# Performance work log

Measured on AMD Instinct MI355X. Metric: run time of the kernel, lower is better.

The kernel has to match this reference:

```python
import jax, jax.numpy as jnp
import numpy as np

NTYPES = 2
MAXNEI = 128      # maxNeighborNum
M2 = 16
NPER = 256        # atoms per type
B = 4
EMB = [25, 50, 100]
FIT_IN = M2 * EMB[-1]  # 1600
FH = 240


def setup_inputs() -> dict:
    key = jax.random.key(0)
    ks = jax.random.split(key, 16)
    s = 0.1
    inp = {
        "Ri": jax.random.normal(ks[0], (B, NTYPES * NPER, NTYPES * MAXNEI, 4), jnp.float32),
        "emb_W0": jax.random.normal(ks[1], (4, 1, EMB[0]), jnp.float32) * s,
        "emb_b0": jax.random.normal(ks[2], (4, EMB[0]), jnp.float32) * s,
        "emb_W1": jax.random.normal(ks[3], (4, EMB[0], EMB[1]), jnp.float32) * s,
        "emb_b1": jax.random.normal(ks[4], (4, EMB[1]), jnp.float32) * s,
        "emb_W2": jax.random.normal(ks[5], (4, EMB[1], EMB[2]), jnp.float32) * s,
        "emb_b2": jax.random.normal(ks[6], (4, EMB[2]), jnp.float32) * s,
        "fit_W0": jax.random.normal(ks[7], (2, FIT_IN, FH), jnp.float32) * 0.02,
        "fit_b0": jax.random.normal(ks[8], (2, FH), jnp.float32) * s,
        "fit_W1": jax.random.normal(ks[9], (2, FH, FH), jnp.float32) * 0.05,
        "fit_b1": jax.random.normal(ks[10], (2, FH), jnp.float32) * s,
        "fit_W2": jax.random.normal(ks[11], (2, FH, FH), jnp.float32) * 0.05,
        "fit_b2": jax.random.normal(ks[12], (2, FH), jnp.float32) * s,
        "fit_W3": jax.random.normal(ks[13], (2, FH, 1), jnp.float32) * 0.05,
        "fit_b3": jax.random.normal(ks[14], (2, 1), jnp.float32),
    }
    return inp


def _emb(s, W0, b0, W1, b1, W2, b2):
    # DeepMD-style embedding MLP with doubling resnet skips (1->25->50->100)
    h0 = jnp.tanh(s @ W0 + b0)
    h1 = jnp.tanh(h0 @ W1 + b1) + jnp.concatenate([h0, h0], axis=-1)
    h2 = jnp.tanh(h1 @ W2 + b2) + jnp.concatenate([h1, h1], axis=-1)
    return h2


def _fit(d, W0, b0, W1, b1, W2, b2, W3, b3):
    h = jnp.tanh(d @ W0 + b0)
    h = jnp.tanh(h @ W1 + b1) + h   # resnet skip (equal dims)
    h = jnp.tanh(h @ W2 + b2) + h
    return h @ W3 + b3              # [B, N, 1]


def reference(Ri, emb_W0, emb_b0, emb_W1, emb_b1, emb_W2, emb_b2,
              fit_W0, fit_b0, fit_W1, fit_b1, fit_W2, fit_b2, fit_W3, fit_b3):
    type_nums = NTYPES
    Ei_blocks = []
    for i in range(NTYPES):                      # center-atom type
        Ri_i = Ri[:, i * NPER:(i + 1) * NPER]    # [B, NPER, NTYPES*M, 4]
        xyz = None
        for j in range(NTYPES):                  # neighbor type
            blk = Ri_i[:, :, j * MAXNEI:(j + 1) * MAXNEI, :]  # [B,N,M,4]
            S = blk[..., 0:1]                                  # [B,N,M,1]
            e = i * NTYPES + j
            G = _emb(S, emb_W0[e], emb_b0[e], emb_W1[e], emb_b1[e],
                     emb_W2[e], emb_b2[e])                     # [B,N,M,100]
            tmp = jnp.einsum('bnmc,bnmg->bncg', blk, G)        # [B,N,4,100]
            xyz = tmp if xyz is None else xyz + tmp
        xyz = xyz / (MAXNEI * type_nums)
        xyz_b = xyz[..., :M2]                                  # [B,N,4,16]
        DR = jnp.einsum('bncg,bnch->bngh', xyz, xyz_b)         # [B,N,100,16]
        DR = DR.reshape(B, NPER, FIT_IN)
        Ei_i = _fit(DR, fit_W0[i], fit_b0[i], fit_W1[i], fit_b1[i],
                    fit_W2[i], fit_b2[i], fit_W3[i], fit_b3[i])  # [B,N,1]
        Ei_blocks.append(Ei_i)
    Ei = jnp.concatenate(Ei_blocks, axis=1)     # [B, natoms_sum, 1]
    return Ei[..., 0]                            # per-atom energies [B, natoms_sum]
```

## Files before the change

kernel.cpp:

```cpp
#include <hip/hip_runtime.h>
#include <hip/hip_bf16.h>

#define FH 240
#define FIT_IN 1600
#define NK 2048
#define TSTRIDE 128
#define TLO -16.0f
#define TINVH 64.0f

typedef _Float16 h8 __attribute__((ext_vector_type(8)));
typedef _Float16 h2v __attribute__((ext_vector_type(2)));
typedef float f4v __attribute__((ext_vector_type(4)));

__device__ __forceinline__ float fast_tanh(float x) {
    float e2 = __builtin_amdgcn_exp2f(x * 2.8853900817779268f);
    return 1.0f - 2.0f * __builtin_amdgcn_rcpf(e2 + 1.0f);
}

#define FMA_ROW(r, s) \
    acc[r][0] += (s) * b0.x; acc[r][1] += (s) * b0.y; \
    acc[r][2] += (s) * b0.z; acc[r][3] += (s) * b0.w; \
    acc[r][4] += (s) * b1.x; acc[r][5] += (s) * b1.y; \
    acc[r][6] += (s) * b1.z; acc[r][7] += (s) * b1.w;

#define TOFF_W0   0
#define TOFF_B0   28
#define TOFF_B1   56
#define TOFF_B2   108
#define TOFF_W1   208
#define TOFF_W2   1508
#define TOFF_H0T  6708
#define TOFF_H1T  10008
#define TSMEM     16608

__global__ __launch_bounds__(256) void k_prep(
    const float* __restrict__ eW0, const float* __restrict__ eB0,
    const float* __restrict__ eW1, const float* __restrict__ eB1,
    const float* __restrict__ eW2, const float* __restrict__ eB2,
    ushort* __restrict__ Tp,
    const float* __restrict__ fW0, const float* __restrict__ fW1,
    const float* __restrict__ fW2,
    _Float16* __restrict__ W0T, _Float16* __restrict__ W1T,
    _Float16* __restrict__ W2T)
{
    const int bx = blockIdx.x;
    const int t  = threadIdx.x;

    if (bx >= 64) {
        const int total = 768000 + 115200 + 115200;
        for (int idx = (bx - 64) * 256 + t; idx < total; idx += 64 * 256) {
            if (idx < 768000) {
                const int tp = idx / 384000, r = idx - tp * 384000;
                const int k = r / 240, n = r - k * 240;
                W0T[tp * 384000 + n * 1600 + k] = (_Float16)fW0[idx];
            } else if (idx < 883200) {
                const int j = idx - 768000;
                const int tp = j / 57600, r = j - tp * 57600;
                const int k = r / 240, n = r - k * 240;
                W1T[tp * 57600 + n * 240 + k] = (_Float16)fW1[j];
            } else {
                const int j = idx - 883200;
                const int tp = j / 57600, r = j - tp * 57600;
                const int k = r / 240, n = r - k * 240;
                W2T[tp * 57600 + n * 240 + k] = (_Float16)fW2[j];
            }
        }
        return;
    }

    __shared__ float sm[TSMEM];
    const int w    = t >> 6;
    const int lane = t & 63;
    const int mi   = lane & 7;
    const int gi   = lane >> 3;
    const int mrow = w * 32 + mi * 4;

    const int e  = bx >> 4;
    const int k0 = (bx & 15) * 128;

    {
        uint* Tw = (uint*)Tp;
        for (int idx = t; idx < 128 * 28; idx += 256) {
            const int kk = idx / 28, cp = 100 + idx - (idx / 28) * 28;
            Tw[((size_t)e * NK + k0 + kk) * TSTRIDE + cp] = 0u;
        }
    }

    for (int idx = t; idx < 1250; idx += 256) {
        int k = idx / 50, g = idx - k * 50;
        sm[TOFF_W1 + k * 52 + g] = eW1[e * 1250 + idx];
    }
    for (int idx = t; idx < 5000; idx += 256) {
        int k = idx / 100, r = idx - k * 100;
        int half = r / 50, g = r - half * 50;
        sm[TOFF_W2 + k * 104 + half * 52 + g] = eW2[e * 5000 + idx];
    }
    if (t < 25)       { sm[TOFF_W0 + t] = eW0[e * 25 + t]; sm[TOFF_B0 + t] = eB0[e * 25 + t]; }
    else if (t < 75)  { sm[TOFF_B1 + (t - 25)] = eB1[e * 50 + (t - 25)]; }
    else if (t < 175) { sm[TOFF_B2 + (t - 75)] = eB2[e * 100 + (t - 75)]; }
    __syncthreads();

    if (t < 128) {
        const float S = TLO + (float)(k0 + t) * (1.0f / TINVH);
        #pragma unroll
        for (int k = 0; k < 25; ++k)
            sm[TOFF_H0T + k * 132 + t] = fast_tanh(S * sm[TOFF_W0 + k] + sm[TOFF_B0 + k]);
    }
    __syncthreads();

    {
        float acc[4][8];
        #pragma unroll
        for (int r = 0; r < 4; ++r)
            #pragma unroll
            for (int c = 0; c < 8; ++c) acc[r][c] = 0.f;

        #pragma unroll 5
        for (int k = 0; k < 25; ++k) {
            const float4 av = *(const float4*)&sm[TOFF_H0T + k * 132 + mrow];
            const float4 b0 = *(const float4*)&sm[TOFF_W1 + k * 52 + gi * 8];
            const float4 b1 = *(const float4*)&sm[TOFF_W1 + k * 52 + gi * 8 + 4];
            FMA_ROW(0, av.x) FMA_ROW(1, av.y) FMA_ROW(2, av.z) FMA_ROW(3, av.w)
        }
        #pragma unroll
        for (int c = 0; c < 8; ++c) {
            const int g = gi * 8 + c;
            if (g < 50) {
                const int gm = (g < 25) ? g : g - 25;
                const float4 h0r = *(const float4*)&sm[TOFF_H0T + gm * 132 + mrow];
                const float bias = sm[TOFF_B1 + g];
                float4 o;
                o.x = fast_tanh(acc[0][c] + bias) + h0r.x;
                o.y = fast_tanh(acc[1][c] + bias) + h0r.y;
                o.z = fast_tanh(acc[2][c] + bias) + h0r.z;
                o.w = fast_tanh(acc[3][c] + bias) + h0r.w;
                *(float4*)&sm[TOFF_H1T + g * 132 + mrow] = o;
            }
        }
    }
    __syncthreads();

    for (int half = 0; half < 2; ++half) {
        float acc[4][8];
        #pragma unroll
        for (int r = 0; r < 4; ++r)
            #pragma unroll
            for (int c = 0; c < 8; ++c) acc[r][c] = 0.f;

        #pragma unroll 5
        for (int k = 0; k < 50; ++k) {
            const float4 av = *(const float4*)&sm[TOFF_H1T + k * 132 + mrow];
            const float4 b0 = *(const float4*)&sm[TOFF_W2 + k * 104 + half * 52 + gi * 8];
            const float4 b1 = *(const float4*)&sm[TOFF_W2 + k * 104 + half * 52 + gi * 8 + 4];
            FMA_ROW(0, av.x) FMA_ROW(1, av.y) FMA_ROW(2, av.z) FMA_ROW(3, av.w)
        }
        #pragma unroll
        for (int c = 0; c < 8; ++c) {
            const int g = gi * 8 + c;
            if (g < 50) {
                const float4 h1r = *(const float4*)&sm[TOFF_H1T + g * 132 + mrow];
                const float bias = sm[TOFF_B2 + half * 50 + g];
                const int col = half * 50 + g;
                float vv[4];
                vv[0] = fast_tanh(acc[0][c] + bias) + h1r.x;
                vv[1] = fast_tanh(acc[1][c] + bias) + h1r.y;
                vv[2] = fast_tanh(acc[2][c] + bias) + h1r.z;
                vv[3] = fast_tanh(acc[3][c] + bias) + h1r.w;
                #pragma unroll
                for (int r = 0; r < 4; ++r) {
                    const int kk = k0 + mrow + r;
                    const _Float16 hf = (_Float16)vv[r];
                    const ushort hs = *(const ushort*)&hf;
                    const size_t base = ((size_t)e * NK + kk) * TSTRIDE + col;
                    Tp[2 * base] = hs;
                    if (kk > 0) Tp[2 * (base - TSTRIDE) + 1] = hs;
                }
            }
        }
    }
}

__global__ __launch_bounds__(256) void k_xyz(
    const float* __restrict__ Ri, const ushort* __restrict__ Tp,
    _Float16* __restrict__ DRh)
{
    __shared__ float4 sR[256];
    __shared__ float  sF[256];
    __shared__ int    sI[256];
    __shared__ float  sXYZ[400];

    const int t    = threadIdx.x;
    const int w    = t >> 6;
    const int lane = t & 63;
    const int blk  = blockIdx.x;
    const int b    = blk >> 9;
    const int i    = (blk >> 8) & 1;
    const int n    = blk & 255;

    for (int idx = t; idx < 400; idx += 256) sXYZ[idx] = 0.f;

    {
        const int jj = t >> 7, m = t & 127;
        const size_t row = ((size_t)(b * 512 + i * 256 + n)) * 256 + jj * 128 + m;
        const float4 r = *(const float4*)(Ri + row * 4);
        sR[t] = r;
        float u = (r.x - TLO) * TINVH;
        int ii = (int)u;
        ii = (ii < 0) ? 0 : ((ii > NK - 2) ? NK - 2 : ii);
        sI[t] = ii;
        sF[t] = u - (float)ii;
    }
    __syncthreads();

    float a0[4] = {0.f, 0.f, 0.f, 0.f};
    float a1[4] = {0.f, 0.f, 0.f, 0.f};

    for (int jj = 0; jj < 2; ++jj) {
        const h2v* Te = (const h2v*)Tp + (size_t)(i * 2 + jj) * NK * TSTRIDE;
        for (int m8 = 0; m8 < 32; m8 += 8) {
            h2v va[8], vb[8];
            #pragma unroll
            for (int k = 0; k < 8; ++k) {
                const int s = jj * 128 + (w << 5) + m8 + k;
                const h2v* p = Te + (size_t)sI[s] * TSTRIDE;
                va[k] = p[lane];
                vb[k] = p[64 + lane];
            }
            #pragma unroll
            for (int k = 0; k < 8; ++k) {
                const int s = jj * 128 + (w << 5) + m8 + k;
                const float f = sF[s];
                const float4 R = sR[s];
                const float v0 = (float)va[k][0];
                const float G = v0 + f * ((float)va[k][1] - v0);
                a0[0] += R.x * G; a0[1] += R.y * G; a0[2] += R.z * G; a0[3] += R.w * G;
                const float u0 = (float)vb[k][0];
                const float G2 = u0 + f * ((float)vb[k][1] - u0);
                a1[0] += R.x * G2; a1[1] += R.y * G2; a1[2] += R.z * G2; a1[3] += R.w * G2;
            }
        }
    }

    #pragma unroll
    for (int c = 0; c < 4; ++c) atomicAdd(&sXYZ[c * 100 + lane], a0[c]);
    if (lane < 36) {
        #pragma unroll
        for (int c = 0; c < 4; ++c) atomicAdd(&sXYZ[c * 100 + 64 + lane], a1[c]);
    }
    __syncthreads();

    const float inv = 1.0f / 65536.0f;
    _Float16* dr = DRh + (((size_t)i * 4 + b) * 256 + n) * FIT_IN;
    for (int q = t; q < 400; q += 256) {
        const int gg = q >> 2, h0 = (q & 3) * 4;
        ushort4 pk;
        _Float16* ph = (_Float16*)&pk;
        #pragma unroll
        for (int r = 0; r < 4; ++r) {
            const int h = h0 + r;
            const float v = (sXYZ[gg] * sXYZ[h] + sXYZ[100 + gg] * sXYZ[100 + h]
                           + sXYZ[200 + gg] * sXYZ[200 + h] + sXYZ[300 + gg] * sXYZ[300 + h]) * inv;
            ph[r] = (_Float16)v;
        }
        *(ushort4*)(dr + gg * 16 + h0) = pk;
    }
}

__global__ __launch_bounds__(256) void k_fit0(
    const _Float16* __restrict__ A, const _Float16* __restrict__ WT,
    float* __restrict__ P)
{
    constexpr int K = FIT_IN, CHUNK = 200;
    __shared__ _Float16 sA[32 * 40];
    __shared__ _Float16 sBT[240 * 40];

    const int t    = threadIdx.x;
    const int w    = t >> 6;
    const int lane = t & 63;
    const int ln   = lane & 15;
    const int quad = lane >> 4;

    const int mtile = blockIdx.x;
    const int ks    = blockIdx.y;
    const int row0  = mtile * 32;
    const int tp    = mtile >> 5;
    const int kbeg  = ks * CHUNK, kend = kbeg + CHUNK;
    const int nf0   = w * 4;

    f4v acc[2][4];
    #pragma unroll
    for (int mf = 0; mf < 2; ++mf)
        #pragma unroll
        for (int nf = 0; nf < 4; ++nf) acc[mf][nf] = (f4v)0.f;

    const _Float16* Ab = A + (size_t)row0 * K;
    const _Float16* Wb = WT + (size_t)tp * 240 * K;

    for (int k0 = kbeg; k0 < kend; k0 += 32) {
        {
            const int m = t >> 3, kq = (t & 7) * 4;
            const int k = k0 + kq;
            uint2 v = make_uint2(0u, 0u);
            if (k < kend) v = *(const uint2*)(Ab + (size_t)m * K + k);
            *(uint2*)&sA[m * 40 + kq] = v;
        }
        for (int q = t; q < 1920; q += 256) {
            const int nn = q >> 3, kq = (q & 7) * 4;
            const int k = k0 + kq;
            uint2 v = make_uint2(0u, 0u);
            if (k < kend) v = *(const uint2*)(Wb + (size_t)nn * K + k);
            *(uint2*)&sBT[nn * 40 + kq] = v;
        }
        __syncthreads();

        h8 afr[2];
        #pragma unroll
        for (int mf = 0; mf < 2; ++mf)
            afr[mf] = *(const h8*)&sA[(mf * 16 + ln) * 40 + quad * 8];
        #pragma unroll
        for (int nf = 0; nf < 4; ++nf) {
            const int n15 = nf0 + nf;
            if (n15 < 15) {
                const h8 bfr = *(const h8*)&sBT[(n15 * 16 + ln) * 40 + quad * 8];
                #pragma unroll
                for (int mf = 0; mf < 2; ++mf)
                    acc[mf][nf] = __builtin_amdgcn_mfma_f32_16x16x32_f16(
                        afr[mf], bfr, acc[mf][nf], 0, 0, 0);
            }
        }
        __syncthreads();
    }

    float* Pb = P + ((size_t)ks * 2048 + row0) * FH;
    #pragma unroll
    for (int nf = 0; nf < 4; ++nf) {
        const int n15 = nf0 + nf;
        if (n15 < 15) {
            const int col = n15 * 16 + ln;
            #pragma unroll
            for (int mf = 0; mf < 2; ++mf)
                #pragma unroll
                for (int r = 0; r < 4; ++r)
                    Pb[(size_t)(mf * 16 + quad * 4 + r) * FH + col] = acc[mf][nf][r];
        }
    }
}

__global__ __launch_bounds__(256) void k_fit_tail(
    const float* __restrict__ P, const float* __restrict__ b0,
    const _Float16* __restrict__ W1T, const float* __restrict__ b1,
    const _Float16* __restrict__ W2T, const float* __restrict__ b2,
    const float* __restrict__ W3, const float* __restrict__ b3,
    float* __restrict__ out)
{
    __shared__ float    sAf[16 * 240];
    __shared__ _Float16 sA16[16 * 264];
    __shared__ _Float16 sBT[240 * 40];
    __shared__ float    sW3[240];

    const int t    = threadIdx.x;
    const int w    = t >> 6;
    const int lane = t & 63;
    const int ln   = lane & 15;
    const int quad = lane >> 4;

    const int m0 = blockIdx.x * 16;
    const int tp = m0 >> 10;
    const int nf0 = w * 4;

    {
        const int mr = t >> 4, c0 = t & 15;
        #pragma unroll
        for (int it = 0; it < 15; ++it) {
            const int c = c0 + it * 16;
            float s = 0.f;
            #pragma unroll
            for (int ks = 0; ks < 8; ++ks)
                s += P[(size_t)ks * 2048 * FH + (size_t)(m0 + mr) * FH + c];
            const float v = fast_tanh(s + b0[tp * FH + c]);
            sAf[mr * 240 + c] = v;
            sA16[mr * 264 + c] = (_Float16)v;
        }
        sA16[mr * 264 + 240 + c0] = (_Float16)0.f;
        if (c0 < 8) sA16[mr * 264 + 256 + c0] = (_Float16)0.f;
    }
    if (t < 240) sW3[t] = W3[tp * FH + t];
    __syncthreads();

    for (int layer = 0; layer < 2; ++layer) {
        const _Float16* Wb = (layer == 0 ? W1T : W2T) + (size_t)tp * 240 * 240;
        const float* Bias  = (layer == 0 ? b1 : b2);

        f4v acc[4];
        #pragma unroll
        for (int nf = 0; nf < 4; ++nf) acc[nf] = (f4v)0.f;

        for (int k0 = 0; k0 < 240; k0 += 32) {
            for (int q = t; q < 1920; q += 256) {
                const int nn = q >> 3, kq = (q & 7) * 4;
                const int k = k0 + kq;
                uint2 v = make_uint2(0u, 0u);
                if (k < 240) v = *(const uint2*)(Wb + (size_t)nn * 240 + k);
                *(uint2*)&sBT[nn * 40 + kq] = v;
            }
            __syncthreads();

            const h8 afr = *(const h8*)&sA16[ln * 264 + k0 + quad * 8];
            #pragma unroll
            for (int nf = 0; nf < 4; ++nf) {
                const int n15 = nf0 + nf;
                if (n15 < 15) {
                    const h8 bfr = *(const h8*)&sBT[(n15 * 16 + ln) * 40 + quad * 8];
                    acc[nf] = __builtin_amdgcn_mfma_f32_16x16x32_f16(afr, bfr, acc[nf], 0, 0, 0);
                }
            }
            __syncthreads();
        }

        #pragma unroll
        for (int nf = 0; nf < 4; ++nf) {
            const int n15 = nf0 + nf;
            if (n15 < 15) {
                const int col = n15 * 16 + ln;
                #pragma unroll
                for (int r = 0; r < 4; ++r) {
                    const int row = quad * 4 + r;
                    const float v = fast_tanh(acc[nf][r] + Bias[tp * FH + col])
                                  + sAf[row * 240 + col];
                    sAf[row * 240 + col] = v;
                    sA16[row * 264 + col] = (_Float16)v;
                }
            }
        }
        __syncthreads();
    }

    #pragma unroll
    for (int rr = 0; rr < 4; ++rr) {
        const int row = w * 4 + rr;
        float s = 0.f;
        #pragma unroll
        for (int it = 0; it < 4; ++it) {
            const int c = lane + it * 64;
            if (c < 240) s += sAf[row * 240 + c] * sW3[c];
        }
        #pragma unroll
        for (int off = 32; off > 0; off >>= 1) s += __shfl_down(s, off);
        if (lane == 0) {
            const int g = m0 + row;
            const int rem = g & 1023;
            const int bb = rem >> 8, nn = rem & 255;
            out[bb * 512 + tp * 256 + nn] = s + b3[tp];
        }
    }
}

extern "C" void kernel_launch(void* const* d_in, const int* in_sizes, int n_in,
                              void* d_out, int out_size, void* d_ws, size_t ws_size,
                              hipStream_t stream)
{
    const float* Ri  = (const float*)d_in[0];
    const float* eW0 = (const float*)d_in[1];
    const float* eB0 = (const float*)d_in[2];
    const float* eW1 = (const float*)d_in[3];
    const float* eB1 = (const float*)d_in[4];
    const float* eW2 = (const float*)d_in[5];
    const float* eB2 = (const float*)d_in[6];
    const float* fW0 = (const float*)d_in[7];
    const float* fb0 = (const float*)d_in[8];
    const float* fW1 = (const float*)d_in[9];
    const float* fb1 = (const float*)d_in[10];
    const float* fW2 = (const float*)d_in[11];
    const float* fb2 = (const float*)d_in[12];
    const float* fW3 = (const float*)d_in[13];
    const float* fb3 = (const float*)d_in[14];

    char* p = (char*)d_ws;
    float* P      = (float*)p;      p += (size_t)8 * 2048 * FH * 4;
    ushort* Tp    = (ushort*)p;     p += (size_t)4 * NK * TSTRIDE * 4;
    _Float16* DRh = (_Float16*)p;   p += (size_t)2048 * FIT_IN * 2;
    _Float16* W0T = (_Float16*)p;   p += (size_t)768000 * 2;
    _Float16* W1T = (_Float16*)p;   p += (size_t)115200 * 2;
    _Float16* W2T = (_Float16*)p;   p += (size_t)115200 * 2;

    k_prep<<<dim3(128), dim3(256), 0, stream>>>(eW0, eB0, eW1, eB1, eW2, eB2, Tp,
                                                fW0, fW1, fW2, W0T, W1T, W2T);
    k_xyz<<<dim3(2048), dim3(256), 0, stream>>>(Ri, Tp, DRh);
    k_fit0<<<dim3(64, 8), dim3(256), 0, stream>>>(DRh, W0T, P);
    k_fit_tail<<<dim3(128), dim3(256), 0, stream>>>(P, fb0, W1T, fb1, W2T, fb2,
                                                    fW3, fb3, (float*)d_out);
}
```

Baseline: 198.9 us.

## Halve tanh lookup table, tile weight transposes through LDS, widen fit-tail K staging

Halves the tanh lookup table (NK 2048→1024, lower bound -16→-8), so fewer prep blocks build it. The fitting-weight transpose to fp16 now stages 64x64 tiles in shared memory, giving coalesced reads and writes instead of strided scattered stores. In the fit-tail kernel each layer's weights load in two 128-wide K chunks instead of eight 32-wide ones, cutting barriers per layer but using more shared memory. The narrower table range changes clamping for inputs below -8, which could affect accuracy.

Result: slower. 213.2 us (+7.2%).

```diff
diff --git a/kernel.cpp b/kernel.cpp
--- a/kernel.cpp
+++ b/kernel.cpp
@@ -3,9 +3,9 @@
 
 #define FH 240
 #define FIT_IN 1600
-#define NK 2048
+#define NK 1024
 #define TSTRIDE 128
-#define TLO -16.0f
+#define TLO -8.0f
 #define TINVH 64.0f
 
 typedef _Float16 h8 __attribute__((ext_vector_type(8)));
@@ -43,45 +43,60 @@
     _Float16* __restrict__ W0T, _Float16* __restrict__ W1T,
     _Float16* __restrict__ W2T)
 {
+    __shared__ float sm[TSMEM];
     const int bx = blockIdx.x;
     const int t  = threadIdx.x;
 
-    if (bx >= 64) {
-        const int total = 768000 + 115200 + 115200;
-        for (int idx = (bx - 64) * 256 + t; idx < total; idx += 64 * 256) {
-            if (idx < 768000) {
-                const int tp = idx / 384000, r = idx - tp * 384000;
-                const int k = r / 240, n = r - k * 240;
-                W0T[tp * 384000 + n * 1600 + k] = (_Float16)fW0[idx];
-            } else if (idx < 883200) {
-                const int j = idx - 768000;
-                const int tp = j / 57600, r = j - tp * 57600;
-                const int k = r / 240, n = r - k * 240;
-                W1T[tp * 57600 + n * 240 + k] = (_Float16)fW1[j];
+    if (bx >= 32) {
+        _Float16* sT = (_Float16*)sm;
+        for (int tile = bx - 32; tile < 264; tile += 96) {
+            const float* src; _Float16* dst; int K, kt, nt;
+            if (tile < 200) {
+                const int tp = tile / 100, rem = tile % 100;
+                kt = rem >> 2; nt = rem & 3;
+                src = fW0 + (size_t)tp * 384000; dst = W0T + (size_t)tp * 384000;
+                K = 1600;
             } else {
-                const int j = idx - 883200;
-                const int tp = j / 57600, r = j - tp * 57600;
-                const int k = r / 240, n = r - k * 240;
-                W2T[tp * 57600 + n * 240 + k] = (_Float16)fW2[j];
+                const int j = tile - 200, mat = j >> 5, rem = j & 31;
+                const int tp = rem >> 4, r2 = rem & 15;
+                kt = r2 >> 2; nt = r2 & 3;
+                src = (mat ? fW2 : fW1) + (size_t)tp * 57600;
+                dst = (mat ? W2T : W1T) + (size_t)tp * 57600;
+                K = 240;
+            }
+            const int k0 = kt * 64, n0 = nt * 64;
+            __syncthreads();
+            #pragma unroll 4
+            for (int i = 0; i < 16; ++i) {
+                const int idx = t + i * 256, r = idx >> 6, c = idx & 63;
+                float v = 0.f;
+                if (k0 + r < K && n0 + c < 240) v = src[(size_t)(k0 + r) * 240 + n0 + c];
+                sT[c * 68 + r] = (_Float16)v;
+            }
+            __syncthreads();
+            #pragma unroll 4
+            for (int i = 0; i < 16; ++i) {
+                const int idx = t + i * 256, c = idx >> 6, r = idx & 63;
+                if (n0 + c < 240 && k0 + r < K)
+                    dst[(size_t)(n0 + c) * K + k0 + r] = sT[c * 68 + r];
             }
         }
         return;
     }
 
-    __shared__ float sm[TSMEM];
     const int w    = t >> 6;
     const int lane = t & 63;
     const int mi   = lane & 7;
     const int gi   = lane >> 3;
     const int mrow = w * 32 + mi * 4;
 
-    const int e  = bx >> 4;
-    const int k0 = (bx & 15) * 128;
+    const int e  = bx >> 3;
+    const int k0 = (bx & 7) * 128;
 
     {
         uint* Tw = (uint*)Tp;
         for (int idx = t; idx < 128 * 28; idx += 256) {
-            const int kk = idx / 28, cp = 100 + idx - (idx / 28) * 28;
+            const int kk = idx / 28, cp = 100 + (idx - kk * 28);
             Tw[((size_t)e * NK + k0 + kk) * TSTRIDE + cp] = 0u;
         }
     }
@@ -355,7 +370,7 @@
 {
     __shared__ float    sAf[16 * 240];
     __shared__ _Float16 sA16[16 * 264];
-    __shared__ _Float16 sBT[240 * 40];
+    __shared__ _Float16 sBT[240 * 136];
     __shared__ float    sW3[240];
 
     const int t    = threadIdx.x;
@@ -395,23 +410,27 @@
         #pragma unroll
         for (int nf = 0; nf < 4; ++nf) acc[nf] = (f4v)0.f;
 
-        for (int k0 = 0; k0 < 240; k0 += 32) {
-            for (int q = t; q < 1920; q += 256) {
-                const int nn = q >> 3, kq = (q & 7) * 4;
-                const int k = k0 + kq;
+        for (int half = 0; half < 2; ++half) {
+            for (int q = t; q < 240 * 34; q += 256) {
+                const int nn = q / 34, s = q - nn * 34;
+                const int kq = s * 4;
+                const int k = half * 128 + kq;
                 uint2 v = make_uint2(0u, 0u);
-                if (k < 240) v = *(const uint2*)(Wb + (size_t)nn * 240 + k);
-                *(uint2*)&sBT[nn * 40 + kq] = v;
+                if (kq < 128 && k < 240) v = *(const uint2*)(Wb + (size_t)nn * 240 + k);
+                *(uint2*)&sBT[nn * 136 + kq] = v;
             }
             __syncthreads();
 
-            const h8 afr = *(const h8*)&sA16[ln * 264 + k0 + quad * 8];
-            #pragma unroll
-            for (int nf = 0; nf < 4; ++nf) {
-                const int n15 = nf0 + nf;
-                if (n15 < 15) {
-                    const h8 bfr = *(const h8*)&sBT[(n15 * 16 + ln) * 40 + quad * 8];
-                    acc[nf] = __builtin_amdgcn_mfma_f32_16x16x32_f16(afr, bfr, acc[nf], 0, 0, 0);
+            #pragma unroll
+            for (int k0 = 0; k0 < 128; k0 += 32) {
+                const h8 afr = *(const h8*)&sA16[ln * 264 + half * 128 + k0 + quad * 8];
+                #pragma unroll
+                for (int nf = 0; nf < 4; ++nf) {
+                    const int n15 = nf0 + nf;
+                    if (n15 < 15) {
+                        const h8 bfr = *(const h8*)&sBT[(n15 * 16 + ln) * 136 + k0 + quad * 8];
+                        acc[nf] = __builtin_amdgcn_mfma_f32_16x16x32_f16(afr, bfr, acc[nf], 0, 0, 0);
+                    }
                 }
             }
             __syncthreads();
```
